# Kernel tuning notes

Hardware: AMD Instinct MI355X
Metric: run time of the kernel (lower is better)

The kernel has to match this reference:

```python
import jax, jax.numpy as jnp
import numpy as np

L = 2          # num_layers
D = 2048       # embed_dim
HQ = 16        # num_q_heads
HK = 4         # num_kv_heads
HD = D // HQ   # head_size = 128
G = HQ // HK   # q_to_kv_ratio = 4
P = 8192       # embed_dim_proj
V = 32000      # vocab_size
B = 1
S = 2048
EPS = 1e-5
THETA = 500000.0
NEG = -1e30


def setup_inputs() -> dict:
    key = jax.random.key(0)
    ks = jax.random.split(key, 8)
    s = 0.02
    return {
        "tokens": jax.random.randint(ks[0], (B, S), 0, V, dtype=jnp.int32),
        "embed": jax.random.normal(ks[1], (V, D), jnp.float32) * s,
        "attn_norm_w": jnp.ones((L, D), jnp.float32),
        "qkv_w": jax.random.normal(ks[2], (L, D, D + 2 * HK * HD), jnp.float32) * s,
        "attn_out_w": jax.random.normal(ks[3], (L, D, D), jnp.float32) * s,
        "mlp_norm_w": jnp.ones((L, D), jnp.float32),
        "mlp_in_w": jax.random.normal(ks[4], (L, D, 2 * P), jnp.float32) * s,
        "mlp_out_w": jax.random.normal(ks[5], (L, P, D), jnp.float32) * s,
        "final_norm_w": jnp.ones((D,), jnp.float32),
        "lm_head_w": jax.random.normal(ks[6], (D, V), jnp.float32) * s,
    }


def _rms(x, w):
    return w * (x * jax.lax.rsqrt(jnp.mean(x * x, axis=-1, keepdims=True) + EPS))


def _rope_cos_sin():
    inv = 1.0 / (THETA ** (jnp.arange(0, HD, 2, dtype=jnp.float32) / HD))  # [HD/2]
    ang = jnp.arange(S, dtype=jnp.float32)[:, None] * inv[None, :]         # [S, HD/2]
    return jnp.cos(ang), jnp.sin(ang)


def _rope(t, cos, sin):
    # t: [B,S,H,HD]; interleaved complex rotation on (even, odd) pairs
    x = t.reshape(t.shape[:-1] + (HD // 2, 2))
    x0, x1 = x[..., 0], x[..., 1]
    c = cos[None, :, None, :]
    sn = sin[None, :, None, :]
    out = jnp.stack([x0 * c - x1 * sn, x0 * sn + x1 * c], axis=-1)
    return out.reshape(t.shape)


def _layer(x, nw1, wqkv, wo, nw2, wi, wmo, cos, sin, mask):
    # attention block (pre-norm, residual)
    h = _rms(x, nw1)
    qkv = h @ wqkv
    q = qkv[..., :D].reshape(B, S, HQ, HD)
    k = qkv[..., D:D + HK * HD].reshape(B, S, HK, HD)
    v = qkv[..., D + HK * HD:].reshape(B, S, HK, HD)
    q = _rope(q, cos, sin)
    k = _rope(k, cos, sin)
    # GQA: repeat_interleave along head dim
    k = jnp.repeat(k, G, axis=2)
    v = jnp.repeat(v, G, axis=2)
    scores = jnp.einsum('bqhd,bkhd->bhqk', q, k) / np.float32(np.sqrt(HD))
    scores = jnp.where(mask, scores, NEG)
    attn = jax.nn.softmax(scores, axis=-1)
    o = jnp.einsum('bhqk,bkhd->bqhd', attn, v).reshape(B, S, D)
    x = x + o @ wo
    # SwiGLU block (pre-norm, residual)
    h = _rms(x, nw2)
    gu = h @ wi
    gate, up = gu[..., :P], gu[..., P:]
    x = x + (jax.nn.silu(gate) * up) @ wmo
    return x


def reference(tokens, embed, attn_norm_w, qkv_w, attn_out_w, mlp_norm_w,
              mlp_in_w, mlp_out_w, final_norm_w, lm_head_w):
    cos, sin = _rope_cos_sin()
    mask = jnp.tril(jnp.ones((S, S), dtype=bool))  # offset=0 prefill -> causal
    x = embed[tokens]  # [B,S,D]
    for i in range(L):
        x = _layer(x, attn_norm_w[i], qkv_w[i], attn_out_w[i],
                   mlp_norm_w[i], mlp_in_w[i], mlp_out_w[i], cos, sin, mask)
    return _rms(x, final_norm_w) @ lm_head_w  # [B,S,V]
```

## Files before the change

kernel.cpp:

```cpp
#include <hip/hip_runtime.h>
#include <math.h>

#define S_LEN 2048
#define DMODEL 2048
#define NHQ 16
#define NHK 4
#define HDIM 128
#define PDIM 8192
#define VOCAB 32000
#define NQKV 3072
#define EPSI 1e-5f

typedef unsigned short u16;
typedef unsigned int u32;
typedef __bf16 bf16x8 __attribute__((ext_vector_type(8)));
typedef float f32x4 __attribute__((ext_vector_type(4)));

__device__ __forceinline__ u16 f2bf(float f){
  u32 u = __builtin_bit_cast(u32, f);
  u += 0x7fffu + ((u >> 16) & 1u);
  return (u16)(u >> 16);
}
__device__ __forceinline__ float bf2f(u16 h){
  u32 u = ((u32)h) << 16;
  return __builtin_bit_cast(float, u);
}
__device__ __forceinline__ bf16x8 ld8(const u16* p){
  return __builtin_bit_cast(bf16x8, *(const uint4*)p);
}
__device__ __forceinline__ f32x4 mfma16(bf16x8 a, bf16x8 b, f32x4 c){
  return __builtin_amdgcn_mfma_f32_16x16x32_bf16(a, b, c, 0, 0, 0);
}

#define GLOAD_LDS16(gp, lp) __builtin_amdgcn_global_load_lds( \
    (__attribute__((address_space(1))) void*)(gp), \
    (__attribute__((address_space(3))) void*)(lp), 16, 0, 0)

__device__ __forceinline__ bf16x8 lds_frag(const u16* Lb, int R, int g){
  const int Rp = R >> 1;
  const int s8 = (((R & 1) << 2) | g) ^ (Rp & 7);
  return ld8(Lb + Rp * 64 + s8 * 8);
}
__device__ __forceinline__ void stage_sw(const u16* base, long row0, int K, int kt,
                                         int q, u16* Ldst_waveuniform){
  const int Rp = q >> 3;
  const int u = (q & 7) ^ (Rp & 7);
  const int R = (Rp << 1) | (u >> 2);
  const u16* gp = base + (row0 + R) * (long)K + kt + ((u & 3) << 3);
  GLOAD_LDS16(gp, Ldst_waveuniform);
}

__global__ void k_embed(const int* __restrict__ tok, const float* __restrict__ emb,
                        float* __restrict__ x){
  const int s = blockIdx.x, t = threadIdx.x;
  const long r = tok[s];
  const float4* src = (const float4*)(emb + r * DMODEL);
  float4* dst = (float4*)(x + (long)s * DMODEL);
  dst[t] = src[t];
  dst[t + 256] = src[t + 256];
}

__global__ void k_rmsnorm(const float* __restrict__ x, const float* __restrict__ w,
                          u16* __restrict__ out){
  const int s = blockIdx.x, t = threadIdx.x;
  const float4* xr = (const float4*)(x + (long)s * DMODEL);
  const float4 a = xr[t], b = xr[t + 256];
  float ss = a.x*a.x + a.y*a.y + a.z*a.z + a.w*a.w
           + b.x*b.x + b.y*b.y + b.z*b.z + b.w*b.w;
  #pragma unroll
  for (int off = 32; off > 0; off >>= 1) ss += __shfl_down(ss, off, 64);
  __shared__ float part[4];
  if ((t & 63) == 0) part[t >> 6] = ss;
  __syncthreads();
  const float r = rsqrtf((part[0] + part[1] + part[2] + part[3]) * (1.f / 2048.f) + EPSI);
  const float4* wr = (const float4*)w;
  const float4 wa = wr[t], wb = wr[t + 256];
  uint2 ua, ub;
  ua.x = (u32)f2bf(a.x*r*wa.x) | ((u32)f2bf(a.y*r*wa.y) << 16);
  ua.y = (u32)f2bf(a.z*r*wa.z) | ((u32)f2bf(a.w*r*wa.w) << 16);
  ub.x = (u32)f2bf(b.x*r*wb.x) | ((u32)f2bf(b.y*r*wb.y) << 16);
  ub.y = (u32)f2bf(b.z*r*wb.z) | ((u32)f2bf(b.w*r*wb.w) << 16);
  *(uint2*)(out + (long)s * DMODEL + 4 * t) = ua;
  *(uint2*)(out + (long)s * DMODEL + 1024 + 4 * t) = ub;
}

__global__ __launch_bounds__(256) void k_convT(const float* __restrict__ W,
                                               u16* __restrict__ Wt, int N, int K){
  const int n0 = blockIdx.x * 64, k0 = blockIdx.y * 64;
  const int t = threadIdx.x;
  __shared__ u16 T[64][72];
  const int r = t >> 4, c = (t & 15) << 2;
  #pragma unroll
  for (int p = 0; p < 4; ++p){
    const int k = p * 16 + r;
    const float4 v = *(const float4*)(W + (long)(k0 + k) * N + n0 + c);
    T[c + 0][k] = f2bf(v.x);
    T[c + 1][k] = f2bf(v.y);
    T[c + 2][k] = f2bf(v.z);
    T[c + 3][k] = f2bf(v.w);
  }
  __syncthreads();
  const int nr = t >> 3, kc = (t & 7) << 3;
  #pragma unroll
  for (int p = 0; p < 2; ++p){
    const int n = p * 32 + nr;
    *(uint4*)(Wt + (long)(n0 + n) * K + k0 + kc) = *(const uint4*)(&T[n][kc]);
  }
}

template<int OUT_BF16, int RES>
__global__ __launch_bounds__(256) void k_gemm(const u16* __restrict__ A, const u16* __restrict__ Bt,
                                              void* C, const float* Rs,
                                              int M, int N, int K){
  const int bm = blockIdx.x, bn = blockIdx.y;
  const int t = threadIdx.x;
  const int w = t >> 6, lane = t & 63, l15 = lane & 15, g = lane >> 4;
  const int wr = w >> 1, wc = w & 1;
  __shared__ u16 As[4096];
  __shared__ u16 Bs[4096];
  f32x4 acc[4][4] = {};
  const long arow = (long)bm * 128;
  const long brow = (long)bn * 128;
  for (int kt = 0; kt < K; kt += 32){
    __syncthreads();
    #pragma unroll
    for (int c = 0; c < 2; ++c){
      const int q0 = ((w << 1) | c) << 6;
      const int q  = q0 | lane;
      stage_sw(A,  arow, K, kt, q, As + q0 * 8);
      stage_sw(Bt, brow, K, kt, q, Bs + q0 * 8);
    }
    __syncthreads();
    bf16x8 af[4], bfr[4];
    #pragma unroll
    for (int i = 0; i < 4; ++i)
      af[i] = lds_frag(As, wr * 64 + i * 16 + l15, g);
    #pragma unroll
    for (int i = 0; i < 4; ++i)
      bfr[i] = lds_frag(Bs, wc * 64 + i * 16 + l15, g);
    #pragma unroll
    for (int mi = 0; mi < 4; ++mi)
      #pragma unroll
      for (int ni = 0; ni < 4; ++ni)
        acc[mi][ni] = mfma16(af[mi], bfr[ni], acc[mi][ni]);
  }
  const int row0 = bm * 128 + wr * 64, col0 = bn * 128 + wc * 64;
  #pragma unroll
  for (int mi = 0; mi < 4; ++mi){
    #pragma unroll
    for (int ni = 0; ni < 4; ++ni){
      #pragma unroll
      for (int r = 0; r < 4; ++r){
        const long ri = row0 + mi * 16 + g * 4 + r;
        const long ci = col0 + ni * 16 + l15;
        float v = acc[mi][ni][r];
        if (RES) v += Rs[ri * N + ci];
        if (OUT_BF16) ((u16*)C)[ri * N + ci] = f2bf(v);
        else          ((float*)C)[ri * N + ci] = v;
      }
    }
  }
}

template<int OUT_BF16>
__global__ __launch_bounds__(512, 2) void k_gemm256(const u16* __restrict__ A,
                                                    const u16* __restrict__ Bt,
                                                    void* C, int M, int N, int K){
  __shared__ u16 L[65536];
  const int t = threadIdx.x;
  const int w = t >> 6, lane = t & 63, l15 = lane & 15, g = lane >> 4;
  const int wr = w >> 2, wc = w & 3;
  const int nbm = M >> 8;
  const int nwg = gridDim.x;
  int id = blockIdx.x;
  {
    const int cpx = nwg >> 3;
    id = (id & 7) * cpx + (id >> 3);
  }
  const int bm = id % nbm, bn = id / nbm;
  const long arow = (long)bm << 8, brow = (long)bn << 8;
  const int NT = K >> 5;

  auto stage_tile = [&](int tile){
    const int sb = (tile & 3) * 8192;
    const int kt = tile << 5;
    #pragma unroll
    for (int i = 0; i < 2; ++i){
      const int q0 = i * 512 + (t & ~63);
      const int q  = i * 512 + t;
      stage_sw(A,  arow, K, kt, q, L + sb + q0 * 8);
      stage_sw(Bt, brow, K, kt, q, L + 32768 + sb + q0 * 8);
    }
  };

  stage_tile(0); stage_tile(1); stage_tile(2);
  asm volatile("s_waitcnt vmcnt(8)" ::: "memory");
  __builtin_amdgcn_s_barrier();

  f32x4 acc[8][4] = {};
  for (int tt = 0; tt < NT; ++tt){
    const u16* sA = L + (tt & 3) * 8192;
    const u16* sB = L + 32768 + (tt & 3) * 8192;
    bf16x8 af[4], bfr[4];
    #pragma unroll
    for (int n = 0; n < 4; ++n)
      bfr[n] = lds_frag(sB, wc * 64 + n * 16 + l15, g);
    #pragma unroll
    for (int j = 0; j < 4; ++j)
      af[j] = lds_frag(sA, wr * 128 + j * 16 + l15, g);
    if (tt + 3 < NT) stage_tile(tt + 3);
    asm volatile("s_waitcnt lgkmcnt(0)" ::: "memory");
    __builtin_amdgcn_s_barrier();
    __builtin_amdgcn_s_setprio(1);
    #pragma unroll
    for (int j = 0; j < 4; ++j)
      #pragma unroll
      for (int n = 0; n < 4; ++n)
        acc[j][n] = mfma16(af[j], bfr[n], acc[j][n]);
    __builtin_amdgcn_s_setprio(0);
    #pragma unroll
    for (int j = 0; j < 4; ++j)
      af[j] = lds_frag(sA, wr * 128 + 64 + j * 16 + l15, g);
    asm volatile("s_waitcnt lgkmcnt(0)" ::: "memory");
    if (tt + 1 < NT){
      if (tt + 3 < NT)      asm volatile("s_waitcnt vmcnt(8)" ::: "memory");
      else if (tt + 2 < NT) asm volatile("s_waitcnt vmcnt(4)" ::: "memory");
      else                  asm volatile("s_waitcnt vmcnt(0)" ::: "memory");
      __builtin_amdgcn_s_barrier();
    }
    __builtin_amdgcn_s_setprio(1);
    #pragma unroll
    for (int j = 0; j < 4; ++j)
      #pragma unroll
      for (int n = 0; n < 4; ++n)
        acc[4 + j][n] = mfma16(af[j], bfr[n], acc[4 + j][n]);
    __builtin_amdgcn_s_setprio(0);
  }
  const int row0 = bm * 256 + wr * 128, col0 = bn * 256 + wc * 64;
  #pragma unroll
  for (int mi = 0; mi < 8; ++mi){
    #pragma unroll
    for (int ni = 0; ni < 4; ++ni){
      #pragma unroll
      for (int r = 0; r < 4; ++r){
        const long ri = row0 + mi * 16 + g * 4 + r;
        const long ci = col0 + ni * 16 + l15;
        const float v = acc[mi][ni][r];
        if (OUT_BF16) ((u16*)C)[ri * N + ci] = f2bf(v);
        else          ((float*)C)[ri * N + ci] = v;
      }
    }
  }
}

__global__ void k_rope(u16* __restrict__ qkv){
  const int idx = blockIdx.x * 256 + threadIdx.x;
  const int i = idx & 63;
  const int head = (idx >> 6) % 20;
  const int s = idx / (64 * 20);
  const long base = (long)s * NQKV + (head < NHQ ? head * HDIM : DMODEL + (head - NHQ) * HDIM);
  u32* p = (u32*)(qkv + base + 2 * i);
  const u32 v = *p;
  const float x0 = bf2f((u16)(v & 0xffffu)), x1 = bf2f((u16)(v >> 16));
  const float ang = (float)s * exp2f(-0.29580575889569023f * (float)i);
  float sn, cs;
  sincosf(ang, &sn, &cs);
  const float y0 = x0 * cs - x1 * sn;
  const float y1 = x0 * sn + x1 * cs;
  *p = (u32)f2bf(y0) | ((u32)f2bf(y1) << 16);
}

__global__ __launch_bounds__(256) void k_attn(const u16* __restrict__ qkv, u16* __restrict__ o){
  const int qb = blockIdx.x, h = blockIdx.y;
  const int kh = h >> 2;
  const int t = threadIdx.x, w = t >> 6, lane = t & 63, l15 = lane & 15, g = lane >> 4;
  __shared__ u16 Ks[64 * 144];
  __shared__ u16 Vt[128 * 80];
  __shared__ u16 Ps[4][16 * 72];
  const int q0 = qb * 64 + w * 16;
  bf16x8 aq[4];
  #pragma unroll
  for (int d0 = 0; d0 < 4; ++d0)
    aq[d0] = ld8(qkv + (long)(q0 + l15) * NQKV + h * HDIM + d0 * 32 + g * 8);
  f32x4 acc_o[8] = {};
  float mst[4], lst[4];
  #pragma unroll
  for (int r = 0; r < 4; ++r){ mst[r] = -1e30f; lst[r] = 0.f; }
  const float scale = 0.08838834764831843f;
  const int krow = t >> 2, kc0 = (t & 3) << 5;
  const int vkv = (t & 31) << 1, vd0 = (t >> 5) << 4;
  for (int kt = 0; kt <= qb; ++kt){
    const int kv0 = kt << 6;
    __syncthreads();
    {
      const u16* kp = qkv + (long)(kv0 + krow) * NQKV + DMODEL + kh * HDIM + kc0;
      u16* kd = Ks + krow * 144 + kc0;
      #pragma unroll
      for (int c = 0; c < 4; ++c)
        *(uint4*)(kd + c * 8) = *(const uint4*)(kp + c * 8);
    }
    {
      const u16* vp = qkv + (long)(kv0 + vkv) * NQKV + DMODEL + 512 + kh * HDIM + vd0;
      const uint4 a0 = *(const uint4*)vp;
      const uint4 a1 = *(const uint4*)(vp + 8);
      const uint4 b0 = *(const uint4*)(vp + NQKV);
      const uint4 b1 = *(const uint4*)(vp + NQKV + 8);
      const u32 aw[8] = {a0.x,a0.y,a0.z,a0.w,a1.x,a1.y,a1.z,a1.w};
      const u32 bw[8] = {b0.x,b0.y,b0.z,b0.w,b1.x,b1.y,b1.z,b1.w};
      #pragma unroll
      for (int i2 = 0; i2 < 8; ++i2){
        *(u32*)(Vt + (vd0 + 2 * i2)     * 80 + vkv) = (aw[i2] & 0xffffu) | ((bw[i2] & 0xffffu) << 16);
        *(u32*)(Vt + (vd0 + 2 * i2 + 1) * 80 + vkv) = (aw[i2] >> 16)     | ((bw[i2] >> 16) << 16);
      }
    }
    __syncthreads();
    f32x4 sacc[4] = {};
    #pragma unroll
    for (int d0 = 0; d0 < 4; ++d0){
      #pragma unroll
      for (int j = 0; j < 4; ++j){
        const bf16x8 bk = ld8(Ks + (j * 16 + l15) * 144 + d0 * 32 + g * 8);
        sacc[j] = mfma16(aq[d0], bk, sacc[j]);
      }
    }
    float p[4][4], scl[4];
    #pragma unroll
    for (int r = 0; r < 4; ++r){
      const int qrow = q0 + g * 4 + r;
      float mx = -1e30f;
      #pragma unroll
      for (int j = 0; j < 4; ++j){
        float sv = sacc[j][r] * scale;
        sv = (kv0 + j * 16 + l15 <= qrow) ? sv : -1e30f;
        p[j][r] = sv;
        mx = fmaxf(mx, sv);
      }
      #pragma unroll
      for (int off = 1; off < 16; off <<= 1) mx = fmaxf(mx, __shfl_xor(mx, off, 64));
      const float mnew = fmaxf(mst[r], mx);
      scl[r] = __expf(mst[r] - mnew);
      float rs = 0.f;
      #pragma unroll
      for (int j = 0; j < 4; ++j){ p[j][r] = __expf(p[j][r] - mnew); rs += p[j][r]; }
      #pragma unroll
      for (int off = 1; off < 16; off <<= 1) rs += __shfl_xor(rs, off, 64);
      lst[r] = lst[r] * scl[r] + rs;
      mst[r] = mnew;
    }
    #pragma unroll
    for (int n = 0; n < 8; ++n)
      #pragma unroll
      for (int r = 0; r < 4; ++r)
        acc_o[n][r] *= scl[r];
    #pragma unroll
    for (int j = 0; j < 4; ++j)
      #pragma unroll
      for (int r = 0; r < 4; ++r)
        Ps[w][(g * 4 + r) * 72 + j * 16 + l15] = f2bf(p[j][r]);
    #pragma unroll
    for (int kk = 0; kk < 2; ++kk){
      const bf16x8 pa = ld8(Ps[w] + l15 * 72 + kk * 32 + g * 8);
      #pragma unroll
      for (int n = 0; n < 8; ++n){
        const bf16x8 bv = ld8(Vt + (n * 16 + l15) * 80 + kk * 32 + g * 8);
        acc_o[n] = mfma16(pa, bv, acc_o[n]);
      }
    }
  }
  #pragma unroll
  for (int n = 0; n < 8; ++n){
    #pragma unroll
    for (int r = 0; r < 4; ++r){
      const float ov = acc_o[n][r] / lst[r];
      o[(long)(q0 + g * 4 + r) * DMODEL + h * HDIM + n * 16 + l15] = f2bf(ov);
    }
  }
}

__global__ void k_swiglu(const u16* __restrict__ gu, u16* __restrict__ out){
  const long idx = ((long)blockIdx.x * 256 + threadIdx.x) * 8;
  const long s = idx >> 13;
  const int j = (int)(idx & 8191);
  const u16* gp = gu + s * 16384 + j;
  const uint4 gv = *(const uint4*)gp;
  const uint4 uv = *(const uint4*)(gp + PDIM);
  const u32 gw[4] = {gv.x, gv.y, gv.z, gv.w};
  const u32 uw[4] = {uv.x, uv.y, uv.z, uv.w};
  u32 ow[4];
  #pragma unroll
  for (int k = 0; k < 4; ++k){
    const float g0 = bf2f((u16)(gw[k] & 0xffffu)), g1 = bf2f((u16)(gw[k] >> 16));
    const float u0 = bf2f((u16)(uw[k] & 0xffffu)), u1 = bf2f((u16)(uw[k] >> 16));
    const float s0 = g0 / (1.f + __expf(-g0)) * u0;
    const float s1 = g1 / (1.f + __expf(-g1)) * u1;
    ow[k] = (u32)f2bf(s0) | ((u32)f2bf(s1) << 16);
  }
  uint4 ro; ro.x = ow[0]; ro.y = ow[1]; ro.z = ow[2]; ro.w = ow[3];
  *(uint4*)(out + idx) = ro;
}

extern "C" void kernel_launch(void* const* d_in, const int* in_sizes, int n_in,
                              void* d_out, int out_size, void* d_ws, size_t ws_size,
                              hipStream_t stream){
  const int*   tokens       = (const int*)d_in[0];
  const float* embed        = (const float*)d_in[1];
  const float* attn_norm_w  = (const float*)d_in[2];
  const float* qkv_w        = (const float*)d_in[3];
  const float* attn_out_w   = (const float*)d_in[4];
  const float* mlp_norm_w   = (const float*)d_in[5];
  const float* mlp_in_w     = (const float*)d_in[6];
  const float* mlp_out_w    = (const float*)d_in[7];
  const float* final_norm_w = (const float*)d_in[8];
  const float* lm_head_w    = (const float*)d_in[9];

  char* ws = (char*)d_ws;
  float* xf  = (float*)(ws);
  u16* hbf   = (u16*)(ws + 16777216);
  u16* qkvb  = (u16*)(ws + 25165824);
  u16* obf   = (u16*)(ws + 37748736);
  u16* gub   = (u16*)(ws + 46137344);
  u16* hb2   = (u16*)(ws + 113246208);
  u16* wbuf  = (u16*)(ws + 146800640);

  k_embed<<<S_LEN, 256, 0, stream>>>(tokens, embed, xf);
  for (int l = 0; l < 2; ++l){
    k_rmsnorm<<<S_LEN, 256, 0, stream>>>(xf, attn_norm_w + (long)l * DMODEL, hbf);
    k_convT<<<dim3(NQKV/64, DMODEL/64), 256, 0, stream>>>(
        qkv_w + (long)l * DMODEL * NQKV, wbuf, NQKV, DMODEL);
    k_gemm<1,0><<<dim3(S_LEN/128, NQKV/128), 256, 0, stream>>>(
        hbf, wbuf, qkvb, nullptr, S_LEN, NQKV, DMODEL);
    k_rope<<<(S_LEN * 20 * 64) / 256, 256, 0, stream>>>(qkvb);
    k_attn<<<dim3(S_LEN/64, NHQ), 256, 0, stream>>>(qkvb, obf);
    k_convT<<<dim3(DMODEL/64, DMODEL/64), 256, 0, stream>>>(
        attn_out_w + (long)l * DMODEL * DMODEL, wbuf, DMODEL, DMODEL);
    k_gemm<0,1><<<dim3(S_LEN/128, DMODEL/128), 256, 0, stream>>>(
        obf, wbuf, xf, xf, S_LEN, DMODEL, DMODEL);
    k_rmsnorm<<<S_LEN, 256, 0, stream>>>(xf, mlp_norm_w + (long)l * DMODEL, hbf);
    k_convT<<<dim3((2*PDIM)/64, DMODEL/64), 256, 0, stream>>>(
        mlp_in_w + (long)l * DMODEL * 2 * PDIM, wbuf, 2*PDIM, DMODEL);
    k_gemm256<1><<<(S_LEN/256) * ((2*PDIM)/256), 512, 0, stream>>>(
        hbf, wbuf, gub, S_LEN, 2*PDIM, DMODEL);
    k_swiglu<<<(S_LEN * PDIM / 8) / 256, 256, 0, stream>>>(gub, hb2);
    k_convT<<<dim3(DMODEL/64, PDIM/64), 256, 0, stream>>>(
        mlp_out_w + (long)l * PDIM * DMODEL, wbuf, DMODEL, PDIM);
    k_gemm<0,1><<<dim3(S_LEN/128, DMODEL/128), 256, 0, stream>>>(
        hb2, wbuf, xf, xf, S_LEN, DMODEL, PDIM);
  }
  k_rmsnorm<<<S_LEN, 256, 0, stream>>>(xf, final_norm_w, hbf);
  k_convT<<<dim3(VOCAB/64, DMODEL/64), 256, 0, stream>>>(lm_head_w, wbuf, VOCAB, DMODEL);
  k_gemm256<0><<<(S_LEN/256) * (VOCAB/256), 512, 0, stream>>>(
      hbf, wbuf, (float*)d_out, S_LEN, VOCAB, DMODEL);
}
```

Before: 1.625 ms.

## Precompute staging pointers and load all A fragments before a single barrier per k-tile

Replaces the per-tile staging lambda with precomputed, incrementing global pointers whose swizzle is computed once. The k-loop now reads all eight A fragments and four B fragments up front, issues the prefetch, and does one wait and barrier before 32 back-to-back MFMAs, instead of two half-phases each with its own barrier. This removes one barrier and the per-tile address arithmetic per k-step. In exchange it holds more fragment registers and gives less interleaving of LDS reads with MFMA work, which may hurt occupancy at two blocks per CU.

```diff
diff --git a/kernel.cpp b/kernel.cpp
--- a/kernel.cpp
+++ b/kernel.cpp
@@ -171,29 +171,34 @@
   const int w = t >> 6, lane = t & 63, l15 = lane & 15, g = lane >> 4;
   const int wr = w >> 2, wc = w & 3;
   const int nbm = M >> 8;
-  const int nwg = gridDim.x;
   int id = blockIdx.x;
   {
-    const int cpx = nwg >> 3;
+    const int cpx = gridDim.x >> 3;
     id = (id & 7) * cpx + (id >> 3);
   }
   const int bm = id % nbm, bn = id / nbm;
-  const long arow = (long)bm << 8, brow = (long)bn << 8;
   const int NT = K >> 5;
 
-  auto stage_tile = [&](int tile){
-    const int sb = (tile & 3) * 8192;
-    const int kt = tile << 5;
-    #pragma unroll
-    for (int i = 0; i < 2; ++i){
-      const int q0 = i * 512 + (t & ~63);
-      const int q  = i * 512 + t;
-      stage_sw(A,  arow, K, kt, q, L + sb + q0 * 8);
-      stage_sw(Bt, brow, K, kt, q, L + 32768 + sb + q0 * 8);
-    }
+  const int Rp0 = t >> 3;
+  const int u0  = (t & 7) ^ (Rp0 & 7);
+  const int R0  = (Rp0 << 1) | (u0 >> 2);
+  const u16* pA0 = A  + ((long)bm * 256 + R0) * (long)K + ((u0 & 3) << 3);
+  const u16* pB0 = Bt + ((long)bn * 256 + R0) * (long)K + ((u0 & 3) << 3);
+  const u16* pA1 = pA0 + (long)128 * K;
+  const u16* pB1 = pB0 + (long)128 * K;
+  const int w0 = (t & ~63) * 8;
+
+  auto stagef = [&](int slot){
+    u16* ldsA = L + slot * 8192;
+    u16* ldsB = L + 32768 + slot * 8192;
+    GLOAD_LDS16(pA0, ldsA + w0);
+    GLOAD_LDS16(pB0, ldsB + w0);
+    GLOAD_LDS16(pA1, ldsA + 4096 + w0);
+    GLOAD_LDS16(pB1, ldsB + 4096 + w0);
+    pA0 += 32; pB0 += 32; pA1 += 32; pB1 += 32;
   };
 
-  stage_tile(0); stage_tile(1); stage_tile(2);
+  stagef(0); stagef(1); stagef(2);
   asm volatile("s_waitcnt vmcnt(8)" ::: "memory");
   __builtin_amdgcn_s_barrier();
 
@@ -201,28 +206,16 @@
   for (int tt = 0; tt < NT; ++tt){
     const u16* sA = L + (tt & 3) * 8192;
     const u16* sB = L + 32768 + (tt & 3) * 8192;
-    bf16x8 af[4], bfr[4];
+    bf16x8 af[8], bfr[4];
+    #pragma unroll
+    for (int j = 0; j < 8; ++j)
+      af[j] = lds_frag(sA, wr * 128 + j * 16 + l15, g);
     #pragma unroll
     for (int n = 0; n < 4; ++n)
       bfr[n] = lds_frag(sB, wc * 64 + n * 16 + l15, g);
-    #pragma unroll
-    for (int j = 0; j < 4; ++j)
-      af[j] = lds_frag(sA, wr * 128 + j * 16 + l15, g);
-    if (tt + 3 < NT) stage_tile(tt + 3);
-    asm volatile("s_waitcnt lgkmcnt(0)" ::: "memory");
-    __builtin_amdgcn_s_barrier();
-    __builtin_amdgcn_s_setprio(1);
-    #pragma unroll
-    for (int j = 0; j < 4; ++j)
-      #pragma unroll
-      for (int n = 0; n < 4; ++n)
-        acc[j][n] = mfma16(af[j], bfr[n], acc[j][n]);
-    __builtin_amdgcn_s_setprio(0);
-    #pragma unroll
-    for (int j = 0; j < 4; ++j)
-      af[j] = lds_frag(sA, wr * 128 + 64 + j * 16 + l15, g);
-    asm volatile("s_waitcnt lgkmcnt(0)" ::: "memory");
+    if (tt + 3 < NT) stagef((tt + 3) & 3);
     if (tt + 1 < NT){
+      asm volatile("s_waitcnt lgkmcnt(0)" ::: "memory");
       if (tt + 3 < NT)      asm volatile("s_waitcnt vmcnt(8)" ::: "memory");
       else if (tt + 2 < NT) asm volatile("s_waitcnt vmcnt(4)" ::: "memory");
       else                  asm volatile("s_waitcnt vmcnt(0)" ::: "memory");
@@ -230,10 +223,10 @@
     }
     __builtin_amdgcn_s_setprio(1);
     #pragma unroll
-    for (int j = 0; j < 4; ++j)
-      #pragma unroll
-      for (int n = 0; n < 4; ++n)
-        acc[4 + j][n] = mfma16(af[j], bfr[n], acc[4 + j][n]);
+    for (int mi = 0; mi < 8; ++mi)
+      #pragma unroll
+      for (int ni = 0; ni < 4; ++ni)
+        acc[mi][ni] = mfma16(af[mi], bfr[ni], acc[mi][ni]);
     __builtin_amdgcn_s_setprio(0);
   }
   const int row0 = bm * 256 + wr * 128, col0 = bn * 256 + wc * 64;
```

Result: no change. 1.602 ms (-1.5%).
